# Performance work log

Measured on AMD Instinct MI355X. Metric: run time of the kernel, lower is better.

The kernel has to match this reference:

```python
import jax, jax.numpy as jnp
import numpy as np

# Quantization constants from the original module
X_ZP = -66   # int8 zero point
Y_ZP = 160   # uint8 zero point


def setup_inputs() -> dict:
    key = jax.random.key(0)
    k1, k2 = jax.random.split(key)
    # x: [7, B, M, K] int8 in [-128, 127]
    x = jax.random.randint(k1, (7, 8, 512, 1024), -128, 128, dtype=jnp.int32).astype(jnp.int8)
    # y: [B, K, N] uint8 in [0, 255]
    y = jax.random.randint(k2, (8, 1024, 512), 0, 256, dtype=jnp.int32).astype(jnp.uint8)
    return {
        "x": x,
        "y": y,
        "x_scale": jnp.float32(0.03),
        "y_scale": jnp.float32(0.025),
    }


def reference(x, y, x_scale, y_scale):
    # dequantize_per_tensor: (q - zero_point) * scale
    xf = (x.astype(jnp.float32) - jnp.float32(X_ZP)) * x_scale   # [7, B, M, K]
    yf = (y.astype(jnp.float32) - jnp.float32(Y_ZP)) * y_scale   # [B, K, N]
    # torch.matmul broadcast: [7,B,M,K] @ [B,K,N] -> [7,B,M,N]
    return jnp.einsum('gbmk,bkn->gbmn', xf, yf)
```

## Files before the change

### kernel.cpp

```cpp
#include <hip/hip_runtime.h>
#include <stdint.h>

#define AS1 __attribute__((address_space(1)))
#define AS3 __attribute__((address_space(3)))

typedef int v4i __attribute__((ext_vector_type(4)));

constexpr int G = 7, B = 8, M = 512, N = 512, K = 1024;
constexpr int GBn = G * B;

constexpr size_t X8_BYTES = (size_t)GBn * M * K;
constexpr size_t YT_BYTES = (size_t)B * N * K;
constexpr size_t RS_CNT   = (size_t)GBn * M;
constexpr size_t CS_CNT   = (size_t)B * N;
constexpr size_t WS_NEEDED = X8_BYTES + YT_BYTES + RS_CNT * 4 + CS_CNT * 4;

__global__ __launch_bounds__(256) void transpose_pack_y(const int* __restrict__ y,
                                                        signed char* __restrict__ yt) {
    __shared__ unsigned char tile[64][80];
    int n0 = blockIdx.x * 64;
    int k0 = blockIdx.y * 64;
    int b  = blockIdx.z;
    int t  = threadIdx.x;

    int r  = t >> 2;
    int c0 = (t & 3) * 16;
    const int* src = y + ((size_t)b * K + k0 + r) * N + n0 + c0;
    uint32_t p[4];
#pragma unroll
    for (int q = 0; q < 4; ++q) {
        int4 v = ((const int4*)src)[q];
        p[q] =  (uint32_t)((v.x & 255) ^ 128)
             | ((uint32_t)((v.y & 255) ^ 128) << 8)
             | ((uint32_t)((v.z & 255) ^ 128) << 16)
             | ((uint32_t)((v.w & 255) ^ 128) << 24);
    }
    *(uint4*)&tile[r][c0] = make_uint4(p[0], p[1], p[2], p[3]);
    __syncthreads();

    int nl = t >> 2;
    int kc = (t & 3) * 16;
    uint32_t q[4];
#pragma unroll
    for (int w = 0; w < 4; ++w) {
        uint32_t b0 = tile[kc + w * 4 + 0][nl];
        uint32_t b1 = tile[kc + w * 4 + 1][nl];
        uint32_t b2 = tile[kc + w * 4 + 2][nl];
        uint32_t b3 = tile[kc + w * 4 + 3][nl];
        q[w] = b0 | (b1 << 8) | (b2 << 16) | (b3 << 24);
    }
    *(uint4*)(yt + ((size_t)b * N + n0 + nl) * K + k0 + kc) = make_uint4(q[0], q[1], q[2], q[3]);
}

__device__ __forceinline__ int wave_reduce_sum(int v) {
#pragma unroll
    for (int off = 32; off > 0; off >>= 1) v += __shfl_down(v, off, 64);
    return v;
}

__global__ __launch_bounds__(256) void pack_x_sums(const int* __restrict__ x,
                                                   signed char* __restrict__ x8,
                                                   const signed char* __restrict__ yt,
                                                   int* __restrict__ rowsum,
                                                   int* __restrict__ colsum) {
    int wave = threadIdx.x >> 6, lane = threadIdx.x & 63;
    int row = blockIdx.x * 4 + wave;
    if (row < (int)(GBn * M)) {
        const int* src = x + (size_t)row * K + lane * 16;
        int s = 0;
        uint32_t p[4];
#pragma unroll
        for (int q = 0; q < 4; ++q) {
            int4 v = ((const int4*)src)[q];
            s += v.x + v.y + v.z + v.w;
            p[q] =  (uint32_t)(v.x & 255)
                 | ((uint32_t)(v.y & 255) << 8)
                 | ((uint32_t)(v.z & 255) << 16)
                 | ((uint32_t)(v.w & 255) << 24);
        }
        *(uint4*)(x8 + (size_t)row * K + lane * 16) = make_uint4(p[0], p[1], p[2], p[3]);
        s = wave_reduce_sum(s);
        if (lane == 0) rowsum[row] = s;
    } else {
        int rr = row - (int)(GBn * M);
        uint4 u = *(const uint4*)(yt + (size_t)rr * K + lane * 16);
        uint32_t wds[4] = {u.x, u.y, u.z, u.w};
        int s = 0;
#pragma unroll
        for (int q = 0; q < 4; ++q) {
            uint32_t w = wds[q];
            s += (int)(signed char)(w) + (int)(signed char)(w >> 8)
               + (int)(signed char)(w >> 16) + (int)(signed char)(w >> 24);
        }
        s = wave_reduce_sum(s);
        if (lane == 0) colsum[rr] = s;
    }
}

__global__ __launch_bounds__(256, 2) void gemm_i8(const signed char* __restrict__ x8,
                                                  const signed char* __restrict__ yt,
                                                  const int* __restrict__ rowsum,
                                                  const int* __restrict__ colsum,
                                                  const float* __restrict__ xsp,
                                                  const float* __restrict__ ysp,
                                                  float* __restrict__ out) {
    __shared__ signed char As[128 * 64];
    __shared__ signed char Bs[128 * 64];

    int tile = blockIdx.x;
    int gb   = blockIdx.y;
    int mt = tile >> 2, nt = tile & 3;
    int b  = gb & 7;
    int tid = threadIdx.x, wave = tid >> 6, lane = tid & 63;
    int wm = (wave >> 1) * 64, wn = (wave & 1) * 64;

    int srow  = lane >> 2;
    int sslot = (lane & 3) ^ ((lane >> 3) & 3);
    const signed char* Ab = x8 + ((size_t)(gb * M + mt * 128 + wave * 32 + srow)) * K + sslot * 16;
    const signed char* Bb = yt + ((size_t)(b  * N + nt * 128 + wave * 32 + srow)) * K + sslot * 16;
    signed char* AsW = As + wave * 2048;
    signed char* BsW = Bs + wave * 2048;

    v4i zero = {0, 0, 0, 0};
    v4i acc[4][4];
#pragma unroll
    for (int i = 0; i < 4; ++i)
#pragma unroll
        for (int j = 0; j < 4; ++j) acc[i][j] = zero;

    int fr = lane & 15;
    int fk = ((lane >> 4) ^ ((fr >> 1) & 3)) * 16;

    for (int k0 = 0; k0 < K; k0 += 64) {
#pragma unroll
        for (int c = 0; c < 2; ++c) {
            __builtin_amdgcn_global_load_lds((const AS1 uint32_t*)(Ab + (size_t)c * 16 * K + k0),
                                             (AS3 uint32_t*)(AsW + c * 1024), 16, 0, 0);
            __builtin_amdgcn_global_load_lds((const AS1 uint32_t*)(Bb + (size_t)c * 16 * K + k0),
                                             (AS3 uint32_t*)(BsW + c * 1024), 16, 0, 0);
        }
        __syncthreads();

        v4i af[4], bf[4];
#pragma unroll
        for (int i = 0; i < 4; ++i)
            af[i] = *(const v4i*)(As + (wm + i * 16 + fr) * 64 + fk);
#pragma unroll
        for (int j = 0; j < 4; ++j)
            bf[j] = *(const v4i*)(Bs + (wn + j * 16 + fr) * 64 + fk);

#pragma unroll
        for (int i = 0; i < 4; ++i)
#pragma unroll
            for (int j = 0; j < 4; ++j)
                acc[i][j] = __builtin_amdgcn_mfma_i32_16x16x64_i8(af[i], bf[j], acc[i][j], 0, 0, 0);
        __syncthreads();
    }

    float s = xsp[0] * ysp[0];
    int colL = lane & 15;
    int rowQ = (lane >> 4) * 4;
    float* outg = out + (size_t)gb * M * N;
    const int* rs = rowsum + gb * M;
    const int* cs = colsum + b * N;
#pragma unroll
    for (int i = 0; i < 4; ++i) {
#pragma unroll
        for (int r = 0; r < 4; ++r) {
            int row_g = mt * 128 + wm + i * 16 + rowQ + r;
            int rsv = rs[row_g];
#pragma unroll
            for (int j = 0; j < 4; ++j) {
                int col_g = nt * 128 + wn + j * 16 + colL;
                int t = acc[i][j][r] - 32 * rsv + 66 * cs[col_g] - 2162688;
                outg[(size_t)row_g * N + col_g] = s * (float)t;
            }
        }
    }
}

__global__ __launch_bounds__(256) void naive_kernel(const int* __restrict__ x,
                                                    const int* __restrict__ y,
                                                    const float* __restrict__ xsp,
                                                    const float* __restrict__ ysp,
                                                    float* __restrict__ out) {
    size_t idx = (size_t)blockIdx.x * 256 + threadIdx.x;
    int n  = (int)(idx & 511);
    int m  = (int)((idx >> 9) & 511);
    int gb = (int)(idx >> 18);
    int b  = gb & 7;
    const int* xr = x + ((size_t)gb * M + m) * K;
    const int* yc = y + (size_t)b * K * N + n;
    int dot = 0, sx = 0, sy = 0;
    for (int k = 0; k < K; ++k) {
        int a = xr[k];
        int c = yc[(size_t)k * N];
        dot += a * c; sx += a; sy += c;
    }
    float s = xsp[0] * ysp[0];
    out[idx] = s * (float)(dot - 160 * sx + 66 * sy - 10813440);
}

extern "C" void kernel_launch(void* const* d_in, const int* in_sizes, int n_in,
                              void* d_out, int out_size, void* d_ws, size_t ws_size,
                              hipStream_t stream) {
    const int*   x  = (const int*)d_in[0];
    const int*   y  = (const int*)d_in[1];
    const float* xs = (const float*)d_in[2];
    const float* ys = (const float*)d_in[3];
    float* out = (float*)d_out;

    if (ws_size < WS_NEEDED) {
        naive_kernel<<<(14680064 + 255) / 256, 256, 0, stream>>>(x, y, xs, ys, out);
        return;
    }

    char* ws = (char*)d_ws;
    signed char* x8 = (signed char*)ws;
    signed char* yt = (signed char*)(ws + X8_BYTES);
    int* rowsum = (int*)(ws + X8_BYTES + YT_BYTES);
    int* colsum = rowsum + RS_CNT;

    transpose_pack_y<<<dim3(N / 64, K / 64, B), 256, 0, stream>>>(y, yt);
    pack_x_sums<<<(GBn * M + CS_CNT) / 4, 256, 0, stream>>>(x, x8, yt, rowsum, colsum);
    gemm_i8<<<dim3(16, GBn), 256, 0, stream>>>(x8, yt, rowsum, colsum, xs, ys, out);
}
```

Before: 226.7 us.

## Fuse x int8 packing and row sums into GEMM with double-buffered full-N tiles

Drops the separate x packing/row-sum kernel: the GEMM now reads the int32 x directly, packs it to int8 in registers, stores it to LDS and accumulates row sums on the fly. Column sums are computed as per-k-tile partials inside the y transpose kernel and reduced in the GEMM. The GEMM moves to 512 threads covering all 512 N columns per 128-row tile, with double-buffered LDS and prefetch of the next k-tile, and a swizzled block order over 224 blocks. This removes a full write and re-read of the packed x in global memory, but uses much more LDS per block and leaves only 224 blocks, which may underfill the GPU.

Result: faster. 216.7 us (-4.4%).

```diff
diff --git a/kernel.cpp b/kernel.cpp
--- a/kernel.cpp
+++ b/kernel.cpp
@@ -9,19 +9,19 @@
 constexpr int G = 7, B = 8, M = 512, N = 512, K = 1024;
 constexpr int GBn = G * B;
 
-constexpr size_t X8_BYTES = (size_t)GBn * M * K;
 constexpr size_t YT_BYTES = (size_t)B * N * K;
-constexpr size_t RS_CNT   = (size_t)GBn * M;
-constexpr size_t CS_CNT   = (size_t)B * N;
-constexpr size_t WS_NEEDED = X8_BYTES + YT_BYTES + RS_CNT * 4 + CS_CNT * 4;
+constexpr size_t CSP_CNT  = (size_t)16 * B * N;
+constexpr size_t WS_NEEDED = YT_BYTES + CSP_CNT * 4;
 
 __global__ __launch_bounds__(256) void transpose_pack_y(const int* __restrict__ y,
-                                                        signed char* __restrict__ yt) {
+                                                        signed char* __restrict__ yt,
+                                                        int* __restrict__ csp) {
     __shared__ unsigned char tile[64][80];
-    int n0 = blockIdx.x * 64;
-    int k0 = blockIdx.y * 64;
-    int b  = blockIdx.z;
-    int t  = threadIdx.x;
+    int n0  = blockIdx.x * 64;
+    int k0t = blockIdx.y;
+    int k0  = k0t * 64;
+    int b   = blockIdx.z;
+    int t   = threadIdx.x;
 
     int r  = t >> 2;
     int c0 = (t & 3) * 16;
@@ -41,139 +41,151 @@
     int nl = t >> 2;
     int kc = (t & 3) * 16;
     uint32_t q[4];
+    int s = 0;
 #pragma unroll
     for (int w = 0; w < 4; ++w) {
         uint32_t b0 = tile[kc + w * 4 + 0][nl];
         uint32_t b1 = tile[kc + w * 4 + 1][nl];
         uint32_t b2 = tile[kc + w * 4 + 2][nl];
         uint32_t b3 = tile[kc + w * 4 + 3][nl];
+        s += (int)(signed char)b0 + (int)(signed char)b1
+           + (int)(signed char)b2 + (int)(signed char)b3;
         q[w] = b0 | (b1 << 8) | (b2 << 16) | (b3 << 24);
     }
     *(uint4*)(yt + ((size_t)b * N + n0 + nl) * K + k0 + kc) = make_uint4(q[0], q[1], q[2], q[3]);
-}
-
-__device__ __forceinline__ int wave_reduce_sum(int v) {
-#pragma unroll
-    for (int off = 32; off > 0; off >>= 1) v += __shfl_down(v, off, 64);
-    return v;
-}
-
-__global__ __launch_bounds__(256) void pack_x_sums(const int* __restrict__ x,
-                                                   signed char* __restrict__ x8,
-                                                   const signed char* __restrict__ yt,
-                                                   int* __restrict__ rowsum,
-                                                   int* __restrict__ colsum) {
-    int wave = threadIdx.x >> 6, lane = threadIdx.x & 63;
-    int row = blockIdx.x * 4 + wave;
-    if (row < (int)(GBn * M)) {
-        const int* src = x + (size_t)row * K + lane * 16;
+
+    s += __shfl_xor(s, 1, 64);
+    s += __shfl_xor(s, 2, 64);
+    if ((t & 3) == 0) csp[(size_t)k0t * (B * N) + b * N + n0 + nl] = s;
+}
+
+__global__ __launch_bounds__(512, 2) void gemm_fused(const int* __restrict__ x,
+                                                     const signed char* __restrict__ yt,
+                                                     const int* __restrict__ csp,
+                                                     const float* __restrict__ xsp,
+                                                     const float* __restrict__ ysp,
+                                                     float* __restrict__ out) {
+    __shared__ __align__(16) signed char As[2][128 * 64];
+    __shared__ __align__(16) signed char Bs[2][512 * 64];
+    __shared__ int cs_lds[512];
+    __shared__ int rs_lds[128];
+
+    int id  = blockIdx.x;
+    int swz = (id & 7) * 28 + (id >> 3);
+    int gb  = swz >> 2;
+    int mt  = swz & 3;
+    int b   = gb & 7;
+
+    int tid = threadIdx.x, wave = tid >> 6, lane = tid & 63;
+
+    {
         int s = 0;
-        uint32_t p[4];
+        const int* p = csp + b * N + tid;
+#pragma unroll
+        for (int kt = 0; kt < 16; ++kt) s += p[(size_t)kt * (B * N)];
+        cs_lds[tid] = s;
+    }
+
+    int arow = tid >> 2;
+    int akq  = tid & 3;
+    const int4* Asrc = (const int4*)(x + ((size_t)(gb * M + mt * 128 + arow)) * K) + akq * 4;
+    int aoff = arow * 64 + ((akq ^ ((arow >> 1) & 3)) << 4);
+
+    int brl    = lane >> 2;
+    int bchunk = (lane & 3) ^ ((lane >> 3) & 3);
+    const signed char* Bsrc = yt + ((size_t)b * N) * K;
+
+    int fr = lane & 15;
+    int fk = ((lane >> 4) ^ ((fr >> 1) & 3)) << 4;
+    int wm = (wave >> 2) * 64;
+    int wn = (wave & 3) * 128;
+
+    v4i zero = {0, 0, 0, 0};
+    v4i acc[4][8];
+#pragma unroll
+    for (int i = 0; i < 4; ++i)
+#pragma unroll
+        for (int j = 0; j < 8; ++j) acc[i][j] = zero;
+
+    int rsum = 0;
+
+    int4 av[4];
+#pragma unroll
+    for (int q = 0; q < 4; ++q) av[q] = Asrc[q];
+#pragma unroll
+    for (int c = 0; c < 4; ++c) {
+        __builtin_amdgcn_global_load_lds(
+            (const AS1 uint32_t*)(Bsrc + (size_t)(c * 128 + wave * 16 + brl) * K + bchunk * 16),
+            (AS3 uint32_t*)(&Bs[0][(c * 128 + wave * 16) * 64]), 16, 0, 0);
+    }
+
+#pragma unroll 2
+    for (int t = 0; t < 16; ++t) {
+        int cur = t & 1;
+
+        uint32_t pw[4];
+        int s = 0;
 #pragma unroll
         for (int q = 0; q < 4; ++q) {
-            int4 v = ((const int4*)src)[q];
+            int4 v = av[q];
             s += v.x + v.y + v.z + v.w;
-            p[q] =  (uint32_t)(v.x & 255)
+            pw[q] =  (uint32_t)(v.x & 255)
                  | ((uint32_t)(v.y & 255) << 8)
                  | ((uint32_t)(v.z & 255) << 16)
                  | ((uint32_t)(v.w & 255) << 24);
         }
-        *(uint4*)(x8 + (size_t)row * K + lane * 16) = make_uint4(p[0], p[1], p[2], p[3]);
-        s = wave_reduce_sum(s);
-        if (lane == 0) rowsum[row] = s;
-    } else {
-        int rr = row - (int)(GBn * M);
-        uint4 u = *(const uint4*)(yt + (size_t)rr * K + lane * 16);
-        uint32_t wds[4] = {u.x, u.y, u.z, u.w};
-        int s = 0;
-#pragma unroll
-        for (int q = 0; q < 4; ++q) {
-            uint32_t w = wds[q];
-            s += (int)(signed char)(w) + (int)(signed char)(w >> 8)
-               + (int)(signed char)(w >> 16) + (int)(signed char)(w >> 24);
+        rsum += s;
+        *(uint4*)(&As[cur][aoff]) = make_uint4(pw[0], pw[1], pw[2], pw[3]);
+
+        __syncthreads();
+
+        v4i af[4], bf[8];
+#pragma unroll
+        for (int i = 0; i < 4; ++i)
+            af[i] = *(const v4i*)(&As[cur][(wm + i * 16 + fr) * 64 + fk]);
+#pragma unroll
+        for (int j = 0; j < 8; ++j)
+            bf[j] = *(const v4i*)(&Bs[cur][(wn + j * 16 + fr) * 64 + fk]);
+
+        if (t < 15) {
+#pragma unroll
+            for (int q = 0; q < 4; ++q) av[q] = Asrc[(t + 1) * 16 + q];
+#pragma unroll
+            for (int c = 0; c < 4; ++c) {
+                __builtin_amdgcn_global_load_lds(
+                    (const AS1 uint32_t*)(Bsrc + (size_t)(c * 128 + wave * 16 + brl) * K
+                                          + (t + 1) * 64 + bchunk * 16),
+                    (AS3 uint32_t*)(&Bs[cur ^ 1][(c * 128 + wave * 16) * 64]), 16, 0, 0);
+            }
         }
-        s = wave_reduce_sum(s);
-        if (lane == 0) colsum[rr] = s;
-    }
-}
-
-__global__ __launch_bounds__(256, 2) void gemm_i8(const signed char* __restrict__ x8,
-                                                  const signed char* __restrict__ yt,
-                                                  const int* __restrict__ rowsum,
-                                                  const int* __restrict__ colsum,
-                                                  const float* __restrict__ xsp,
-                                                  const float* __restrict__ ysp,
-                                                  float* __restrict__ out) {
-    __shared__ signed char As[128 * 64];
-    __shared__ signed char Bs[128 * 64];
-
-    int tile = blockIdx.x;
-    int gb   = blockIdx.y;
-    int mt = tile >> 2, nt = tile & 3;
-    int b  = gb & 7;
-    int tid = threadIdx.x, wave = tid >> 6, lane = tid & 63;
-    int wm = (wave >> 1) * 64, wn = (wave & 1) * 64;
-
-    int srow  = lane >> 2;
-    int sslot = (lane & 3) ^ ((lane >> 3) & 3);
-    const signed char* Ab = x8 + ((size_t)(gb * M + mt * 128 + wave * 32 + srow)) * K + sslot * 16;
-    const signed char* Bb = yt + ((size_t)(b  * N + nt * 128 + wave * 32 + srow)) * K + sslot * 16;
-    signed char* AsW = As + wave * 2048;
-    signed char* BsW = Bs + wave * 2048;
-
-    v4i zero = {0, 0, 0, 0};
-    v4i acc[4][4];
-#pragma unroll
-    for (int i = 0; i < 4; ++i)
-#pragma unroll
-        for (int j = 0; j < 4; ++j) acc[i][j] = zero;
-
-    int fr = lane & 15;
-    int fk = ((lane >> 4) ^ ((fr >> 1) & 3)) * 16;
-
-    for (int k0 = 0; k0 < K; k0 += 64) {
-#pragma unroll
-        for (int c = 0; c < 2; ++c) {
-            __builtin_amdgcn_global_load_lds((const AS1 uint32_t*)(Ab + (size_t)c * 16 * K + k0),
-                                             (AS3 uint32_t*)(AsW + c * 1024), 16, 0, 0);
-            __builtin_amdgcn_global_load_lds((const AS1 uint32_t*)(Bb + (size_t)c * 16 * K + k0),
-                                             (AS3 uint32_t*)(BsW + c * 1024), 16, 0, 0);
-        }
-        __syncthreads();
-
-        v4i af[4], bf[4];
+
 #pragma unroll
         for (int i = 0; i < 4; ++i)
-            af[i] = *(const v4i*)(As + (wm + i * 16 + fr) * 64 + fk);
-#pragma unroll
-        for (int j = 0; j < 4; ++j)
-            bf[j] = *(const v4i*)(Bs + (wn + j * 16 + fr) * 64 + fk);
-
-#pragma unroll
-        for (int i = 0; i < 4; ++i)
-#pragma unroll
-            for (int j = 0; j < 4; ++j)
+#pragma unroll
+            for (int j = 0; j < 8; ++j)
                 acc[i][j] = __builtin_amdgcn_mfma_i32_16x16x64_i8(af[i], bf[j], acc[i][j], 0, 0, 0);
-        __syncthreads();
-    }
-
-    float s = xsp[0] * ysp[0];
+    }
+
+    rsum += __shfl_xor(rsum, 1, 64);
+    rsum += __shfl_xor(rsum, 2, 64);
+    if ((tid & 3) == 0) rs_lds[arow] = rsum;
+    __syncthreads();
+
+    float sc = xsp[0] * ysp[0];
     int colL = lane & 15;
     int rowQ = (lane >> 4) * 4;
-    float* outg = out + (size_t)gb * M * N;
-    const int* rs = rowsum + gb * M;
-    const int* cs = colsum + b * N;
+    float* outg = out + (size_t)gb * (M * N) + (size_t)(mt * 128) * N;
 #pragma unroll
     for (int i = 0; i < 4; ++i) {
 #pragma unroll
         for (int r = 0; r < 4; ++r) {
-            int row_g = mt * 128 + wm + i * 16 + rowQ + r;
-            int rsv = rs[row_g];
-#pragma unroll
-            for (int j = 0; j < 4; ++j) {
-                int col_g = nt * 128 + wn + j * 16 + colL;
-                int t = acc[i][j][r] - 32 * rsv + 66 * cs[col_g] - 2162688;
-                outg[(size_t)row_g * N + col_g] = s * (float)t;
+            int row_l = wm + i * 16 + rowQ + r;
+            int rsv = rs_lds[row_l];
+#pragma unroll
+            for (int j = 0; j < 8; ++j) {
+                int col = wn + j * 16 + colL;
+                int tv = acc[i][j][r] - 32 * rsv + 66 * cs_lds[col] - 2162688;
+                outg[(size_t)row_l * N + col] = sc * (float)tv;
             }
         }
     }
@@ -216,12 +228,9 @@
     }
 
     char* ws = (char*)d_ws;
-    signed char* x8 = (signed char*)ws;
-    signed char* yt = (signed char*)(ws + X8_BYTES);
-    int* rowsum = (int*)(ws + X8_BYTES + YT_BYTES);
-    int* colsum = rowsum + RS_CNT;
-
-    transpose_pack_y<<<dim3(N / 64, K / 64, B), 256, 0, stream>>>(y, yt);
-    pack_x_sums<<<(GBn * M + CS_CNT) / 4, 256, 0, stream>>>(x, x8, yt, rowsum, colsum);
-    gemm_i8<<<dim3(16, GBn), 256, 0, stream>>>(x8, yt, rowsum, colsum, xs, ys, out);
-}
+    signed char* yt  = (signed char*)ws;
+    int*         csp = (int*)(ws + YT_BYTES);
+
+    transpose_pack_y<<<dim3(N / 64, K / 64, B), 256, 0, stream>>>(y, yt, csp);
+    gemm_fused<<<dim3(224), 512, 0, stream>>>(x, yt, csp, xs, ys, out);
+}
```
